# Kernel tuning notes

Hardware: AMD Instinct MI355X
Metric: run time of the kernel (lower is better)

Reference implementation:

```python
import jax, jax.numpy as jnp
import numpy as np

NUM_LOW, NUM_HIGH, DIM = 8192, 1024, 2048
EPS = 1e-10


def sparsemax(z):
    # z: [..., K]; Martins & Astudillo sparsemax along last axis.
    K = z.shape[-1]
    z_sorted = jnp.flip(jnp.sort(z, axis=-1), axis=-1)          # descending
    z_cum = jnp.cumsum(z_sorted, axis=-1)
    k = jnp.arange(1, K + 1, dtype=z.dtype)
    support = (1.0 + k * z_sorted) > z_cum                       # bool [..., K]
    k_sup = jnp.sum(support, axis=-1, keepdims=True)             # int [..., 1]
    tau = (jnp.take_along_axis(z_cum, k_sup - 1, axis=-1) - 1.0) / k_sup.astype(z.dtype)
    return jnp.maximum(z - tau, 0.0)


def normalize_rows(x, eps=EPS):
    return x / (jnp.sum(x, axis=1, keepdims=True) + eps)


def setup_inputs() -> dict:
    key = jax.random.key(0)
    k1, k2, k3, k4 = jax.random.split(key, 4)

    def xavier(k, shape):
        bound = float(np.sqrt(6.0 / (shape[0] + shape[1])))
        return jax.random.uniform(k, shape, jnp.float32, -bound, bound)

    return {
        "low_w": xavier(k1, (NUM_LOW, DIM)),    # low Concepts parameter
        "high_w": xavier(k2, (NUM_HIGH, DIM)),  # high Concepts parameter
        "Wq": xavier(k3, (DIM, DIM)),           # q_linear.weight (keep_head_dim, n_head=1)
        "Wk": xavier(k4, (DIM, DIM)),           # k_linear.weight
        "norm_low_concepts": 1,
        "norm_high_concepts": 1,
    }


def reference(low_w, high_w, Wq, Wk, norm_low_concepts, norm_high_concepts):
    # Concepts modules: return (possibly normalized) concepts + cosine similarity.
    low_normed = low_w / jnp.linalg.norm(low_w, axis=1, keepdims=True)
    low_concepts = low_normed if norm_low_concepts else low_w
    low_cos = low_normed @ low_normed.T                          # [NL, NL]

    high_normed = high_w / jnp.linalg.norm(high_w, axis=1, keepdims=True)
    high_concepts = high_normed if norm_high_concepts else high_w
    high_cos = high_normed @ high_normed.T                       # [NH, NH]

    # detach_low_concepts=True -> queries do not receive gradients
    low_q = jax.lax.stop_gradient(low_concepts)

    # ModifiedMultiHeadAttention (n_head=1, keep_head_dim -> d_head=DIM; eval mode,
    # so smooth_max is identity and sparsemax is deterministic).
    q = low_q @ Wq.T                                             # [NL, D]
    k = high_concepts @ Wk.T                                     # [NH, D]
    scale = 1.0 / jnp.sqrt(jnp.asarray(DIM, q.dtype))
    attn = sparsemax((q @ k.T) * scale)                          # [NL, NH]
    high_related_low = attn @ high_concepts                      # [NL, D]

    # output_high_concepts_type == "high_plus_low": add back aggregated low concepts
    aggregated_low = normalize_rows(attn.T) @ low_q              # [NH, D]
    output_high_concepts = high_related_low + attn @ aggregated_low  # [NL, D]

    return (low_concepts, low_cos, output_high_concepts, high_cos, attn)
```

## Files before the change

### kernel.cpp

```cpp
#include <hip/hip_runtime.h>
#include <hip/hip_bf16.h>
#include <stdint.h>

#define NL   8192
#define NHI  1024
#define DIMV 2048

typedef __attribute__((ext_vector_type(8))) short short8;
typedef __attribute__((ext_vector_type(4))) float f32x4;

__device__ __forceinline__ unsigned short f2bf(float x){
  unsigned u = __float_as_uint(x);
  u += 0x7FFFu + ((u >> 16) & 1u);
  return (unsigned short)(u >> 16);
}
__device__ __forceinline__ float bf2f(unsigned short b){
  return __uint_as_float(((unsigned)b) << 16);
}
__device__ __forceinline__ unsigned pack2bf(float a, float b){
  return (unsigned)f2bf(a) | ((unsigned)f2bf(b) << 16);
}

__device__ __forceinline__ void gload16(const void* g, void* l){
  __builtin_amdgcn_global_load_lds(
      (const __attribute__((address_space(1))) unsigned int*)g,
      (__attribute__((address_space(3))) unsigned int*)l, 16, 0, 0);
}

__global__ __launch_bounds__(256)
void prep_kernel(const float* __restrict__ low_w, const float* __restrict__ high_w,
                 const float* __restrict__ Wq, const float* __restrict__ Wk,
                 float* __restrict__ out_lowc, unsigned short* __restrict__ lowN,
                 unsigned short* __restrict__ highN,
                 unsigned short* __restrict__ WqT, unsigned short* __restrict__ WkT){
  __shared__ __align__(16) char smem[8448];
  int id = blockIdx.x;
  if(id < 9216){
    const float* W; float* oF; unsigned short* oB; int row;
    if(id < 8192){ W = low_w; oF = out_lowc; oB = lowN; row = id; }
    else         { W = high_w; oF = nullptr; oB = highN; row = id - 8192; }
    const float* r = W + (size_t)row * DIMV;
    int base = threadIdx.x * 8;
    float4 x0 = *(const float4*)(r + base);
    float4 x1 = *(const float4*)(r + base + 4);
    float ss = x0.x*x0.x + x0.y*x0.y + x0.z*x0.z + x0.w*x0.w
             + x1.x*x1.x + x1.y*x1.y + x1.z*x1.z + x1.w*x1.w;
    #pragma unroll
    for(int s = 1; s < 64; s <<= 1) ss += __shfl_xor(ss, s, 64);
    float* red = (float*)smem;
    if((threadIdx.x & 63) == 0) red[threadIdx.x >> 6] = ss;
    __syncthreads();
    float tot = red[0] + red[1] + red[2] + red[3];
    float inv = 1.0f / sqrtf(tot);
    float y0=x0.x*inv, y1=x0.y*inv, y2=x0.z*inv, y3=x0.w*inv;
    float y4=x1.x*inv, y5=x1.y*inv, y6=x1.z*inv, y7=x1.w*inv;
    if(oF){
      float* o = oF + (size_t)row * DIMV + base;
      *(float4*)o       = make_float4(y0,y1,y2,y3);
      *(float4*)(o + 4) = make_float4(y4,y5,y6,y7);
    }
    uint4 u;
    u.x = pack2bf(y0,y1); u.y = pack2bf(y2,y3);
    u.z = pack2bf(y4,y5); u.w = pack2bf(y6,y7);
    *(uint4*)(oB + (size_t)row * DIMV + base) = u;
  } else {
    id -= 9216;
    const float* in; unsigned short* outp;
    if(id < 1024){ in = Wq; outp = WqT; } else { in = Wk; outp = WkT; id -= 1024; }
    unsigned short (*tile)[65] = (unsigned short(*)[65])smem;
    int tx = id & 31, ty = id >> 5;
    int c0 = tx * 64, r0 = ty * 64;
    int t = threadIdx.x;
    int ci = t & 63, r4 = t >> 6;
    #pragma unroll
    for(int k = 0; k < 16; k++){
      int r = k * 4 + r4;
      tile[r][ci] = f2bf(in[(size_t)(r0 + r) * 2048 + c0 + ci]);
    }
    __syncthreads();
    #pragma unroll
    for(int k = 0; k < 16; k++){
      int cc = k * 4 + r4;
      outp[(size_t)(c0 + cc) * 2048 + r0 + ci] = tile[ci][cc];
    }
  }
}

__device__ __forceinline__ void gemm_core(
    const unsigned short* __restrict__ A, const unsigned short* __restrict__ Bt,
    float* __restrict__ Cf, unsigned short* __restrict__ Cb,
    int M, int N, int K, float scale, int mBase, int nBase,
    int kStart, int kChunk, int outBf16, int mirror, char* smem){
  unsigned short* sA = (unsigned short*)smem;
  unsigned short* sB = sA + 128 * 64;
  int tid = threadIdx.x, lane = tid & 63, wid = tid >> 6;
  int chRow = lane >> 3;
  int chCol = (lane & 7) * 8;
  int wm = wid >> 1, wn = wid & 1;

  f32x4 acc[4][4];
  #pragma unroll
  for(int i=0;i<4;i++)
    #pragma unroll
    for(int j=0;j<4;j++) acc[i][j] = (f32x4){0.f,0.f,0.f,0.f};

  for(int k0 = kStart; k0 < kStart + kChunk; k0 += 64){
    #pragma unroll
    for(int i = 0; i < 4; i++){
      int ch = wid * 4 + i;
      int arow = ch * 8 + chRow;
      gload16(A  + (size_t)(mBase + arow) * K + k0 + chCol, &sA[ch * 512]);
      gload16(Bt + (size_t)(nBase + arow) * K + k0 + chCol, &sB[ch * 512]);
    }
    __syncthreads();
    #pragma unroll
    for(int kk = 0; kk < 64; kk += 32){
      short8 a[4], b[4];
      int krd = kk + (lane >> 4) * 8;
      #pragma unroll
      for(int i = 0; i < 4; i++){
        int row = wm * 64 + i * 16 + (lane & 15);
        a[i] = *reinterpret_cast<const short8*>(&sA[row * 64 + krd]);
        int col = wn * 64 + i * 16 + (lane & 15);
        b[i] = *reinterpret_cast<const short8*>(&sB[col * 64 + krd]);
      }
      #pragma unroll
      for(int i = 0; i < 4; i++)
        #pragma unroll
        for(int j = 0; j < 4; j++)
          acc[i][j] = __builtin_amdgcn_mfma_f32_16x16x32_bf16(a[i], b[j], acc[i][j], 0, 0, 0);
    }
    __syncthreads();
  }

  #pragma unroll
  for(int i = 0; i < 4; i++){
    #pragma unroll
    for(int j = 0; j < 4; j++){
      int row = mBase + wm * 64 + i * 16 + (lane >> 4) * 4;
      int col = nBase + wn * 64 + j * 16 + (lane & 15);
      #pragma unroll
      for(int r = 0; r < 4; r++){
        float v = acc[i][j][r] * scale;
        size_t off = (size_t)(row + r) * N + col;
        if(outBf16) Cb[off] = f2bf(v);
        else        Cf[off] = v;
      }
    }
  }

  if(mirror && mBase != nBase){
    float* tf = (float*)smem;
    #pragma unroll
    for(int rq = 0; rq < 4; rq++){
      int qm = rq >> 1, qn = rq & 1;
      __syncthreads();
      if(wm == qm && wn == qn){
        #pragma unroll
        for(int i = 0; i < 4; i++)
          #pragma unroll
          for(int j = 0; j < 4; j++){
            int rl = i * 16 + (lane >> 4) * 4;
            int cl = j * 16 + (lane & 15);
            #pragma unroll
            for(int r = 0; r < 4; r++)
              tf[(rl + r) * 65 + cl] = acc[i][j][r] * scale;
          }
      }
      __syncthreads();
      int mr = tid >> 2, seg = tid & 3;
      size_t obase = (size_t)(nBase + qn * 64 + mr) * N + mBase + qm * 64 + seg * 16;
      #pragma unroll
      for(int k4 = 0; k4 < 4; k4++){
        float4 v;
        v.x = tf[(seg * 16 + k4 * 4 + 0) * 65 + mr];
        v.y = tf[(seg * 16 + k4 * 4 + 1) * 65 + mr];
        v.z = tf[(seg * 16 + k4 * 4 + 2) * 65 + mr];
        v.w = tf[(seg * 16 + k4 * 4 + 3) * 65 + mr];
        *(float4*)(Cf + obase + k4 * 4) = v;
      }
    }
  }
}

template<int OUT_BF16>
__global__ __launch_bounds__(256, 2)
void gemm_bt_kernel(const unsigned short* __restrict__ A,
                    const unsigned short* __restrict__ Bt,
                    float* __restrict__ Cf, unsigned short* __restrict__ Cb,
                    int M, int N, int K, float scale){
  __shared__ __align__(16) char smem[32768];
  int gx = gridDim.x, gy = gridDim.y;
  int nwg = gx * gy;
  int id = blockIdx.y * gx + blockIdx.x;
  if((nwg & 7) == 0){ int cpx = nwg >> 3; id = (id & 7) * cpx + (id >> 3); }
  int mBase = (id / gx) * 128, nBase = (id % gx) * 128;
  int kChunk = K / (int)gridDim.z;
  int kStart = kChunk * (int)blockIdx.z;
  if(!OUT_BF16) Cf += (size_t)blockIdx.z * M * N;
  gemm_core(A, Bt, Cf, Cb, M, N, K, scale, mBase, nBase, kStart, kChunk, OUT_BF16, 0, smem);
}

__global__ __launch_bounds__(256, 2)
void mega1_kernel(const unsigned short* __restrict__ lowN, float* __restrict__ out_lowcos,
                  const unsigned short* __restrict__ WqT, const unsigned short* __restrict__ WkT,
                  unsigned short* __restrict__ G,
                  const unsigned short* __restrict__ highN, float* __restrict__ hcPart){
  __shared__ __align__(16) char smem[32768];
  int bid = blockIdx.x;
  if(bid < 2080){
    int id = (bid & 7) * 260 + (bid >> 3);
    int Si = 0, rem = id;
    for(;;){ int rl = 10 + 16*(15 - Si); if(rem < rl) break; rem -= rl; Si++; }
    int bi, bj;
    if(rem < 10){
      int ti = 0;
      while((ti+1)*4 - (((ti+1)*ti) >> 1) <= rem) ti++;
      int off = ti*4 - ((ti*(ti-1)) >> 1);
      int tj = ti + (rem - off);
      bi = Si*4 + ti; bj = Si*4 + tj;
    } else {
      int r2 = rem - 10;
      int Sj = Si + 1 + (r2 >> 4);
      int t = r2 & 15;
      bi = Si*4 + (t >> 2); bj = Sj*4 + (t & 3);
    }
    gemm_core(lowN, lowN, out_lowcos, nullptr, NL, NL, DIMV, 1.0f,
              bi*128, bj*128, 0, DIMV, 0, 1, smem);
  } else if(bid < 2336){
    int id2 = bid - 2080;
    int s = (id2 & 7) * 32 + (id2 >> 3);
    gemm_core(WqT, WkT, nullptr, G, DIMV, DIMV, DIMV, 1.0f,
              (s >> 4)*128, (s & 15)*128, 0, DIMV, 1, 0, smem);
  } else {
    int id3 = bid - 2336;
    int z = id3 >> 6, w = id3 & 63;
    int s = (w & 7) * 8 + (w >> 3);
    gemm_core(highN, highN, hcPart + (size_t)z * 1048576, nullptr, NHI, NHI, DIMV, 1.0f,
              (s >> 3)*128, (s & 7)*128, z*1024, 1024, 0, 0, smem);
  }
}

__global__ __launch_bounds__(256, 2)
void megaagg_kernel(const unsigned short* __restrict__ lowNT,
                    const unsigned short* __restrict__ attnT, float* __restrict__ aggP,
                    const float* __restrict__ part, float* __restrict__ colsum){
  __shared__ __align__(16) char smem[32768];
  int bid = blockIdx.x;
  if(bid < 256){
    int z = bid >> 7, w = bid & 127;
    int s = (w & 7) * 16 + (w >> 3);
    gemm_core(lowNT, attnT, aggP + (size_t)z * 2097152, nullptr, DIMV, NHI, NL, 1.0f,
              (s >> 3)*128, (s & 7)*128, z*4096, 4096, 0, 0, smem);
  } else {
    int c = (bid - 256) * 256 + threadIdx.x;
    float s = 0.f;
    for(int i = 0; i < 256; i++) s += part[(size_t)i * NHI + c];
    colsum[c] = s;
  }
}

__global__ __launch_bounds__(256)
void sparsemax_kernel(float* __restrict__ S, unsigned short* __restrict__ attnBf,
                      const float* __restrict__ hcPart, float* __restrict__ out_highcos){
  int bid = blockIdx.x;
  if(bid >= 2048){
    size_t i = ((size_t)(bid - 2048) * 256 + threadIdx.x) * 8;
    float4 a0 = *(const float4*)(hcPart + i);
    float4 a1 = *(const float4*)(hcPart + i + 4);
    float4 b0 = *(const float4*)(hcPart + 1048576 + i);
    float4 b1 = *(const float4*)(hcPart + 1048576 + i + 4);
    *(float4*)(out_highcos + i)     = make_float4(a0.x+b0.x, a0.y+b0.y, a0.z+b0.z, a0.w+b0.w);
    *(float4*)(out_highcos + i + 4) = make_float4(a1.x+b1.x, a1.y+b1.y, a1.z+b1.z, a1.w+b1.w);
    return;
  }
  int wid = threadIdx.x >> 6, lane = threadIdx.x & 63;
  int row = bid * 4 + wid;
  float* z = S + (size_t)row * NHI;
  float v[16];
  #pragma unroll
  for(int j = 0; j < 16; j++) v[j] = z[j * 64 + lane];
  float mx = v[0];
  #pragma unroll
  for(int j = 1; j < 16; j++) mx = fmaxf(mx, v[j]);
  #pragma unroll
  for(int s = 1; s < 64; s <<= 1) mx = fmaxf(mx, __shfl_xor(mx, s, 64));
  float lo = mx - 1.0f, hi = mx;
  for(int it = 0; it < 40; it++){
    float mid = 0.5f * (lo + hi);
    float sum = 0.f;
    #pragma unroll
    for(int j = 0; j < 16; j++) sum += fmaxf(v[j] - mid, 0.f);
    #pragma unroll
    for(int s = 1; s < 64; s <<= 1) sum += __shfl_xor(sum, s, 64);
    if(sum >= 1.0f) lo = mid; else hi = mid;
  }
  float cnt = 0.f, ssum = 0.f;
  #pragma unroll
  for(int j = 0; j < 16; j++){
    if(v[j] > lo){ cnt += 1.f; ssum += v[j]; }
  }
  #pragma unroll
  for(int s = 1; s < 64; s <<= 1){
    cnt  += __shfl_xor(cnt,  s, 64);
    ssum += __shfl_xor(ssum, s, 64);
  }
  float tau = (ssum - 1.0f) / cnt;
  #pragma unroll
  for(int j = 0; j < 16; j++){
    float a = fmaxf(v[j] - tau, 0.f);
    z[j * 64 + lane] = a;
    attnBf[(size_t)row * NHI + j * 64 + lane] = f2bf(a);
  }
}

__global__ __launch_bounds__(256)
void transpose3_kernel(const unsigned short* __restrict__ attnB, unsigned short* __restrict__ attnT,
                       const unsigned short* __restrict__ lowN,  unsigned short* __restrict__ lowNT,
                       const unsigned short* __restrict__ highN, unsigned short* __restrict__ highNT,
                       const float* __restrict__ attnF, float* __restrict__ part){
  int id = blockIdx.x;
  if(id >= 6656){
    int chunk = id - 6656;
    int t = threadIdx.x;
    const float* p = attnF + (size_t)chunk * 32 * NHI;
    float a0=0,a1=0,a2=0,a3=0;
    for(int r = 0; r < 32; r++){
      a0 += p[(size_t)r*NHI + t];
      a1 += p[(size_t)r*NHI + t + 256];
      a2 += p[(size_t)r*NHI + t + 512];
      a3 += p[(size_t)r*NHI + t + 768];
    }
    float* q = part + (size_t)chunk * NHI;
    q[t]=a0; q[t+256]=a1; q[t+512]=a2; q[t+768]=a3;
    return;
  }
  __shared__ unsigned short tile[64][65];
  const unsigned short* in; unsigned short* out; int R, C, tx, ty;
  if(id < 2048){        in = attnB; out = attnT;  R = NL;  C = NHI;  tx = id & 15; ty = id >> 4; }
  else if(id < 6144){ id -= 2048;
                        in = lowN;  out = lowNT;  R = NL;  C = DIMV; tx = id & 31; ty = id >> 5; }
  else {              id -= 6144;
                        in = highN; out = highNT; R = NHI; C = DIMV; tx = id & 31; ty = id >> 5; }
  int c0 = tx * 64, r0 = ty * 64;
  int t = threadIdx.x;
  int ci = t & 63, r4 = t >> 6;
  #pragma unroll
  for(int k = 0; k < 16; k++){
    int r = k * 4 + r4;
    tile[r][ci] = in[(size_t)(r0 + r) * C + c0 + ci];
  }
  __syncthreads();
  #pragma unroll
  for(int k = 0; k < 16; k++){
    int cc = k * 4 + r4;
    out[(size_t)(c0 + cc) * R + r0 + ci] = tile[ci][cc];
  }
}

__global__ __launch_bounds__(256)
void mt_kernel(const unsigned short* __restrict__ highNT, const float* __restrict__ aggP,
               const float* __restrict__ colsum, unsigned short* __restrict__ Mt){
  int idx = blockIdx.x * 256 + threadIdx.x;
  int h = idx & 1023;
  float s = aggP[idx] + aggP[idx + 2097152];
  float val = bf2f(highNT[idx]) + s / (colsum[h] + 1e-10f);
  Mt[idx] = f2bf(val);
}

extern "C" void kernel_launch(void* const* d_in, const int* in_sizes, int n_in,
                              void* d_out, int out_size, void* d_ws, size_t ws_size,
                              hipStream_t stream){
  const float* low_w  = (const float*)d_in[0];
  const float* high_w = (const float*)d_in[1];
  const float* Wq     = (const float*)d_in[2];
  const float* Wk     = (const float*)d_in[3];
  float* out = (float*)d_out;

  char* ws = (char*)d_ws;
  unsigned short* lowN  = (unsigned short*)(ws);
  float*          aggP  = (float*)(ws);
  unsigned short* highN = (unsigned short*)(ws + 33554432);
  unsigned short* WqT   = (unsigned short*)(ws + 37748736);
  unsigned short* WkT   = (unsigned short*)(ws + 46137344);
  unsigned short* attnB = (unsigned short*)(ws + 37748736);
  unsigned short* G     = (unsigned short*)(ws + 54525952);
  unsigned short* R2t   = (unsigned short*)(ws + 62914560);
  unsigned short* lowNT = (unsigned short*)(ws + 54525952);
  float*          part  = (float*)(ws + 88080384);
  float*          colsum= (float*)(ws + 88080384 + 1048576);
  unsigned short* attnT = (unsigned short*)(ws + 92274688);
  float*          hcPart= (float*)(ws + 109051904);
  unsigned short* Mt    = (unsigned short*)(ws + 109051904);
  unsigned short* highNT= (unsigned short*)(ws + 113246208);

  float* out_lowc    = out;
  float* out_lowcos  = out + 16777216;
  float* out_high    = out + 83886080;
  float* out_highcos = out + 100663296;
  float* out_attn    = out + 101711872;

  const float scl = 1.0f / sqrtf((float)DIMV);

  prep_kernel<<<11264, 256, 0, stream>>>(low_w, high_w, Wq, Wk,
                                         out_lowc, lowN, highN, WqT, WkT);
  mega1_kernel<<<2464, 256, 0, stream>>>(lowN, out_lowcos, WqT, WkT, G, highN, hcPart);
  gemm_bt_kernel<1><<<dim3(16,8), 256, 0, stream>>>(highN, G, nullptr, R2t,
                                                    NHI, DIMV, DIMV, 1.0f);
  gemm_bt_kernel<0><<<dim3(8,64), 256, 0, stream>>>(lowN, R2t, out_attn, nullptr,
                                                    NL, NHI, DIMV, scl);
  sparsemax_kernel<<<2560, 256, 0, stream>>>(out_attn, attnB, hcPart, out_highcos);
  transpose3_kernel<<<6912, 256, 0, stream>>>(attnB, attnT, lowN, lowNT, highN, highNT,
                                              out_attn, part);
  megaagg_kernel<<<260, 256, 0, stream>>>(lowNT, attnT, aggP, part, colsum);
  mt_kernel<<<8192, 256, 0, stream>>>(highNT, aggP, colsum, Mt);
  gemm_bt_kernel<0><<<dim3(16,64), 256, 0, stream>>>(attnB, Mt, out_high, nullptr,
                                                     NL, DIMV, NHI, 1.0f);
}
```

Before: 546.7 us.

## Reassociate score chain to compute K=highN·Wk^T before multiplying by Wq

Instead of forming the 2048x2048 product G = Wq^T·Wk and then highN·G, the code now computes k = highN·Wk^T (1024x2048) inside mega1 and then k·Wq to get R2t. This removes a DIM^3 GEMM in favour of a NHI·DIM^2 one, cutting FLOPs in the mega1 stage. Wk is now only converted to bf16 without transposition, and Wq keeps its transpose path. Rounding order changes slightly because the intermediate in bf16 is now k rather than G.

```diff
diff --git a/kernel.cpp b/kernel.cpp
--- a/kernel.cpp
+++ b/kernel.cpp
@@ -32,7 +32,7 @@
                  const float* __restrict__ Wq, const float* __restrict__ Wk,
                  float* __restrict__ out_lowc, unsigned short* __restrict__ lowN,
                  unsigned short* __restrict__ highN,
-                 unsigned short* __restrict__ WqT, unsigned short* __restrict__ WkT){
+                 unsigned short* __restrict__ WqT, unsigned short* __restrict__ WkB){
   __shared__ __align__(16) char smem[8448];
   int id = blockIdx.x;
   if(id < 9216){
@@ -63,10 +63,8 @@
     u.x = pack2bf(y0,y1); u.y = pack2bf(y2,y3);
     u.z = pack2bf(y4,y5); u.w = pack2bf(y6,y7);
     *(uint4*)(oB + (size_t)row * DIMV + base) = u;
-  } else {
+  } else if(id < 10240){
     id -= 9216;
-    const float* in; unsigned short* outp;
-    if(id < 1024){ in = Wq; outp = WqT; } else { in = Wk; outp = WkT; id -= 1024; }
     unsigned short (*tile)[65] = (unsigned short(*)[65])smem;
     int tx = id & 31, ty = id >> 5;
     int c0 = tx * 64, r0 = ty * 64;
@@ -75,14 +73,23 @@
     #pragma unroll
     for(int k = 0; k < 16; k++){
       int r = k * 4 + r4;
-      tile[r][ci] = f2bf(in[(size_t)(r0 + r) * 2048 + c0 + ci]);
+      tile[r][ci] = f2bf(Wq[(size_t)(r0 + r) * 2048 + c0 + ci]);
     }
     __syncthreads();
     #pragma unroll
     for(int k = 0; k < 16; k++){
       int cc = k * 4 + r4;
-      outp[(size_t)(c0 + cc) * 2048 + r0 + ci] = tile[ci][cc];
-    }
+      WqT[(size_t)(c0 + cc) * 2048 + r0 + ci] = tile[ci][cc];
+    }
+  } else {
+    id -= 10240;
+    size_t i = ((size_t)id * 256 + threadIdx.x) * 8;
+    float4 x0 = *(const float4*)(Wk + i);
+    float4 x1 = *(const float4*)(Wk + i + 4);
+    uint4 u;
+    u.x = pack2bf(x0.x,x0.y); u.y = pack2bf(x0.z,x0.w);
+    u.z = pack2bf(x1.x,x1.y); u.w = pack2bf(x1.z,x1.w);
+    *(uint4*)(WkB + i) = u;
   }
 }
 
@@ -203,9 +210,8 @@
 
 __global__ __launch_bounds__(256, 2)
 void mega1_kernel(const unsigned short* __restrict__ lowN, float* __restrict__ out_lowcos,
-                  const unsigned short* __restrict__ WqT, const unsigned short* __restrict__ WkT,
-                  unsigned short* __restrict__ G,
-                  const unsigned short* __restrict__ highN, float* __restrict__ hcPart){
+                  const unsigned short* __restrict__ highN, float* __restrict__ hcPart,
+                  const unsigned short* __restrict__ WkB, unsigned short* __restrict__ kB){
   __shared__ __align__(16) char smem[32768];
   int bid = blockIdx.x;
   if(bid < 2080){
@@ -227,17 +233,17 @@
     }
     gemm_core(lowN, lowN, out_lowcos, nullptr, NL, NL, DIMV, 1.0f,
               bi*128, bj*128, 0, DIMV, 0, 1, smem);
-  } else if(bid < 2336){
+  } else if(bid < 2208){
     int id2 = bid - 2080;
-    int s = (id2 & 7) * 32 + (id2 >> 3);
-    gemm_core(WqT, WkT, nullptr, G, DIMV, DIMV, DIMV, 1.0f,
-              (s >> 4)*128, (s & 15)*128, 0, DIMV, 1, 0, smem);
-  } else {
-    int id3 = bid - 2336;
-    int z = id3 >> 6, w = id3 & 63;
+    int z = id2 >> 6, w = id2 & 63;
     int s = (w & 7) * 8 + (w >> 3);
     gemm_core(highN, highN, hcPart + (size_t)z * 1048576, nullptr, NHI, NHI, DIMV, 1.0f,
               (s >> 3)*128, (s & 7)*128, z*1024, 1024, 0, 0, smem);
+  } else {
+    int id3 = bid - 2208;
+    int s = (id3 & 7) * 16 + (id3 >> 3);
+    gemm_core(highN, WkB, nullptr, kB, NHI, DIMV, DIMV, 1.0f,
+              (s >> 4)*128, (s & 15)*128, 0, DIMV, 1, 0, smem);
   }
 }
 
@@ -382,9 +388,9 @@
   float*          aggP  = (float*)(ws);
   unsigned short* highN = (unsigned short*)(ws + 33554432);
   unsigned short* WqT   = (unsigned short*)(ws + 37748736);
-  unsigned short* WkT   = (unsigned short*)(ws + 46137344);
+  unsigned short* WkB   = (unsigned short*)(ws + 46137344);
   unsigned short* attnB = (unsigned short*)(ws + 37748736);
-  unsigned short* G     = (unsigned short*)(ws + 54525952);
+  unsigned short* kB    = (unsigned short*)(ws + 54525952);
   unsigned short* R2t   = (unsigned short*)(ws + 62914560);
   unsigned short* lowNT = (unsigned short*)(ws + 54525952);
   float*          part  = (float*)(ws + 88080384);
@@ -402,10 +408,10 @@
 
   const float scl = 1.0f / sqrtf((float)DIMV);
 
-  prep_kernel<<<11264, 256, 0, stream>>>(low_w, high_w, Wq, Wk,
-                                         out_lowc, lowN, highN, WqT, WkT);
-  mega1_kernel<<<2464, 256, 0, stream>>>(lowN, out_lowcos, WqT, WkT, G, highN, hcPart);
-  gemm_bt_kernel<1><<<dim3(16,8), 256, 0, stream>>>(highN, G, nullptr, R2t,
+  prep_kernel<<<12288, 256, 0, stream>>>(low_w, high_w, Wq, Wk,
+                                         out_lowc, lowN, highN, WqT, WkB);
+  mega1_kernel<<<2336, 256, 0, stream>>>(lowN, out_lowcos, highN, hcPart, WkB, kB);
+  gemm_bt_kernel<1><<<dim3(16,8), 256, 0, stream>>>(kB, WqT, nullptr, R2t,
                                                     NHI, DIMV, DIMV, 1.0f);
   gemm_bt_kernel<0><<<dim3(8,64), 256, 0, stream>>>(lowN, R2t, out_attn, nullptr,
                                                     NL, NHI, DIMV, scl);
```

New measurement: 547.1 us. Within noise of the previous version (+0.1%).
